# Performance work log

Hardware: AMD Instinct MI355X
Metric: run time of the kernel (lower is better)

## Reference

```python
import jax, jax.numpy as jnp
import numpy as np

TOP_K = 8
ROUTED_SCALING = 2.5


def setup_inputs() -> dict:
    key = jax.random.key(0)
    ks = jax.random.split(key, 8)
    B, S, H, E, I = 2, 1024, 2048, 32, 1024
    IS = 2 * I  # shared expert intermediate (n_shared_experts * moe_intermediate_size)
    w = lambda k, shape: jax.random.normal(k, shape, dtype=jnp.float32) * 0.02
    return {
        "hidden_states": jax.random.normal(ks[0], (B, S, H), dtype=jnp.float32),
        "gate_weight": w(ks[1], (E, H)),
        "w_gate": w(ks[2], (E, H, I)),
        "w_up": w(ks[3], (E, H, I)),
        "w_down": w(ks[4], (E, I, H)),
        "ws_gate": w(ks[5], (H, IS)),
        "ws_up": w(ks[6], (H, IS)),
        "ws_down": w(ks[7], (IS, H)),
    }


def reference(hidden_states, gate_weight, w_gate, w_up, w_down, ws_gate, ws_up, ws_down):
    B, S, H = hidden_states.shape
    x = hidden_states.reshape(-1, H)  # [T, H]
    T = x.shape[0]
    E = gate_weight.shape[0]

    # --- gate (DeepseekV3 top-k router: sigmoid scores, top-k, renormalize, scale) ---
    scores = jax.nn.sigmoid(x @ gate_weight.T)              # [T, E]
    topk_w, topk_i = jax.lax.top_k(scores, TOP_K)           # [T, K]
    topk_w = topk_w / (jnp.sum(topk_w, axis=-1, keepdims=True) + 1e-20)
    topk_w = topk_w * ROUTED_SCALING

    # dense [T, E] combine weights (scatter of top-k weights; zeros elsewhere)
    dense_w = jnp.zeros((T, E), dtype=topk_w.dtype).at[
        jnp.arange(T)[:, None], topk_i
    ].add(topk_w)

    # --- all experts on all tokens (calibrate_all_experts semantics; non-selected get weight 0) ---
    g = jnp.einsum('th,ehi->eti', x, w_gate)                # [E, T, I]
    u = jnp.einsum('th,ehi->eti', x, w_up)                  # [E, T, I]
    eo = jnp.einsum('eti,eih->eth', jax.nn.silu(g) * u, w_down)  # [E, T, H]
    routed = jnp.einsum('eth,te->th', eo, dense_w)          # weighted scatter-combine

    # --- shared expert (gated SiLU MLP on residual) ---
    shared = (jax.nn.silu(x @ ws_gate) * (x @ ws_up)) @ ws_down

    return (routed + shared).reshape(B, S, H)
```

## Files before the change

kernel.cpp:

```cpp
#include <hip/hip_runtime.h>

#define T_TOK 2048
#define H_DIM 2048
#define E_NUM 32
#define I_DIM 1024
#define IS_DIM 2048
#define K_TOT (E_NUM * I_DIM + IS_DIM)
#define SLOT_CAP 2048
#define NE_ALL 34
#define GU_TILES 192
#define DN_TILES 176
#define ACT_SLOTS 24576

typedef __bf16 bf16x8 __attribute__((ext_vector_type(8)));
typedef float  f32x4  __attribute__((ext_vector_type(4)));
static_assert(sizeof(bf16x8) == 16, "bf16x8 must be 16B");

#define OFF_CNT   ((size_t)0)
#define OFF_NTGU  ((size_t)192)
#define OFF_NTDN  ((size_t)196)
#define OFF_BASE  ((size_t)256)
#define OFF_TGU   ((size_t)512)
#define OFF_TDN   ((size_t)1280)
#define OFF_PAIRS ((size_t)2048)
#define OFF_XB    ((size_t)280576)
#define OFF_WGT   ((size_t)8669184)
#define OFF_WUT   ((size_t)142886912)
#define OFF_WSGT  ((size_t)277104640)
#define OFF_WSUT  ((size_t)285493248)
#define OFF_WDT   ((size_t)293881856)
#define OFF_ACT   ((size_t)436488192)

__device__ __forceinline__ unsigned short f2bf(float f) {
  unsigned int u = __float_as_uint(f);
  u += 0x7fffu + ((u >> 16) & 1u);
  return (unsigned short)(u >> 16);
}

__device__ __forceinline__ void gld16(const void* g, void* l) {
  __builtin_amdgcn_global_load_lds(
      (const __attribute__((address_space(1))) unsigned int*)g,
      (__attribute__((address_space(3))) unsigned int*)l, 16, 0, 0);
}

__global__ __launch_bounds__(256) void router_kernel(
    const float* __restrict__ x, const float* __restrict__ gw,
    int* __restrict__ cnt, unsigned int* __restrict__ pairs)
{
  const int t = blockIdx.x;
  __shared__ float xs[H_DIM];
  __shared__ float sc[E_NUM];
  const float4* xr = (const float4*)(x + (long)t * H_DIM);
  for (int i = threadIdx.x; i < H_DIM / 4; i += 256) ((float4*)xs)[i] = xr[i];
  __syncthreads();
  const int e = threadIdx.x >> 3, p = threadIdx.x & 7;
  const float4* ga = (const float4*)(gw + (long)e * H_DIM);
  const float4* xa = (const float4*)xs;
  float s = 0.f;
  #pragma unroll 4
  for (int i = p * 64; i < p * 64 + 64; ++i) {
    float4 a = ga[i], b = xa[i];
    s += a.x * b.x + a.y * b.y + a.z * b.z + a.w * b.w;
  }
  s += __shfl_down(s, 4, 8);
  s += __shfl_down(s, 2, 8);
  s += __shfl_down(s, 1, 8);
  if (p == 0) sc[e] = 1.f / (1.f + expf(-s));
  __syncthreads();
  if (threadIdx.x == 0) {
    float v[E_NUM];
    #pragma unroll
    for (int i = 0; i < E_NUM; ++i) v[i] = sc[i];
    unsigned mask = 0; float sum = 0.f;
    int sel[8]; float wv[8];
    for (int k = 0; k < 8; ++k) {
      float best = -1.f; int bi = 0;
      for (int i = 0; i < E_NUM; ++i)
        if (!((mask >> i) & 1u) && v[i] > best) { best = v[i]; bi = i; }
      mask |= 1u << bi; sel[k] = bi; wv[k] = best; sum += best;
    }
    const float scale = 2.5f / (sum + 1e-20f);
    for (int k = 0; k < 8; ++k) {
      const int slot = atomicAdd(&cnt[sel[k]], 1);
      if (slot < SLOT_CAP) {
        const unsigned int w16 = (unsigned int)f2bf(wv[k] * scale);
        pairs[sel[k] * SLOT_CAP + slot] = (w16 << 16) | (unsigned int)t;
      }
    }
  }
}

__global__ __launch_bounds__(256) void build_tiles_kernel(
    int* __restrict__ cnt, int* __restrict__ base,
    unsigned int* __restrict__ tgu, int* __restrict__ ntgu,
    unsigned int* __restrict__ tdn, int* __restrict__ ntdn,
    unsigned int* __restrict__ pairs)
{
  const int t = threadIdx.x;
  for (int s = t; s < T_TOK; s += 256) {
    const unsigned int pv = (0x3F80u << 16) | (unsigned int)s;
    pairs[32 * SLOT_CAP + s] = pv;
    pairs[33 * SLOT_CAP + s] = pv;
  }
  if (t == 0) {
    cnt[32] = T_TOK; cnt[33] = T_TOK;
    int b = 0, ngu = 0, ndn = 0;
    for (int e = 0; e < NE_ALL; ++e) {
      const int c = (e < 32) ? cnt[e] : T_TOK;
      base[e] = b;
      for (int m0 = 0; m0 < c; m0 += 128) {
        tgu[ngu++] = ((unsigned int)e << 16) | (unsigned int)m0;
        if (e < 33) tdn[ndn++] = ((unsigned int)e << 16) | (unsigned int)m0;
      }
      b += (c + 127) & ~127;
    }
    *ntgu = ngu; *ntdn = ndn;
  }
}

__global__ __launch_bounds__(256) void cvt_bf16_kernel(
    const float* __restrict__ in, unsigned short* __restrict__ out, int n4)
{
  int i = blockIdx.x * 256 + threadIdx.x;
  if (i >= n4) return;
  float4 v = ((const float4*)in)[i];
  ushort4 o;
  o.x = f2bf(v.x); o.y = f2bf(v.y); o.z = f2bf(v.z); o.w = f2bf(v.w);
  ((ushort4*)out)[i] = o;
}

struct TDescTable {
  const float* in[6];
  unsigned short* out[6];
  int C[6];
  int ldout[6];
  long in_bs[6];
  long out_bs[6];
  int nbx[6];
  int nbxy[6];
  int start[7];
};

__global__ __launch_bounds__(256) void transpose_fused(TDescTable td)
{
  const int bid = blockIdx.x;
  int i = 0;
  while (i < 5 && bid >= td.start[i + 1]) ++i;
  const int local = bid - td.start[i];
  const int bz = local / td.nbxy[i];
  const int rem = local % td.nbxy[i];
  const int by = rem / td.nbx[i];
  const int bx = rem % td.nbx[i];
  const float* in = td.in[i] + (long)bz * td.in_bs[i];
  unsigned short* out = td.out[i] + (long)bz * td.out_bs[i];
  const int C = td.C[i], ldout = td.ldout[i];

  __shared__ unsigned short tile[64][258];
  const int c0 = bx * 64;
  const int r0 = by * 256;
  const int t = threadIdx.x;
  const int rl0 = t >> 4;
  const int cl0 = (t & 15) * 4;
  #pragma unroll
  for (int p = 0; p < 16; ++p) {
    const int rl = p * 16 + rl0;
    float4 v = *(const float4*)(in + (long)(r0 + rl) * C + c0 + cl0);
    tile[cl0 + 0][rl] = f2bf(v.x);
    tile[cl0 + 1][rl] = f2bf(v.y);
    tile[cl0 + 2][rl] = f2bf(v.z);
    tile[cl0 + 3][rl] = f2bf(v.w);
  }
  __syncthreads();
  const int cw = t >> 5;
  const int rw = (t & 31) * 8;
  #pragma unroll
  for (int q = 0; q < 8; ++q) {
    const int cl = q * 8 + cw;
    const char* src = (const char*)&tile[cl][rw];
    uint4 o;
    o.x = *(const unsigned int*)(src + 0);
    o.y = *(const unsigned int*)(src + 4);
    o.z = *(const unsigned int*)(src + 8);
    o.w = *(const unsigned int*)(src + 12);
    *(uint4*)(out + (long)(c0 + cl) * ldout + r0 + rw) = o;
  }
}

__global__ __launch_bounds__(512, 4) void gate_up_moe_kernel(
    const unsigned short* __restrict__ xb,
    const unsigned short* __restrict__ bgT,
    const unsigned short* __restrict__ buT,
    const unsigned short* __restrict__ sgT,
    const unsigned short* __restrict__ suT,
    const int* __restrict__ cnt,
    const int* __restrict__ base,
    const unsigned int* __restrict__ pairs,
    const unsigned int* __restrict__ tiles,
    const int* __restrict__ ntp,
    unsigned short* __restrict__ act)
{
  const int ti = blockIdx.y;
  if (ti >= *ntp) return;
  const unsigned int tile = tiles[ti];
  const int e  = (int)(tile >> 16);
  const int m0 = (int)(tile & 0xFFFFu);
  const int cnte = cnt[e];
  const int be = base[e];
  const int n0 = blockIdx.x * 64;
  const long panel = (long)I_DIM * H_DIM;
  const unsigned short* Bg =
      ((e < 32) ? bgT + e * panel : sgT + (e - 32) * panel) + (long)n0 * H_DIM;
  const unsigned short* Bu =
      ((e < 32) ? buT + e * panel : suT + (e - 32) * panel) + (long)n0 * H_DIM;

  __shared__ unsigned short sA[2][128 * 64];
  __shared__ unsigned short sBg[2][64 * 64];
  __shared__ unsigned short sBu[2][64 * 64];

  const int tid = threadIdx.x;
  const int lane = tid & 63;
  const int wid = tid >> 6;
  const int wm = wid >> 1, wn = wid & 1;
  const int l15 = lane & 15;
  const int lk  = (lane >> 4) * 8;
  const int srow = tid >> 3;
  const int scol = (tid & 7) * 8;
  const int scolsw = (((tid & 7) ^ (srow & 7))) * 8;
  const int ksw = (l15 & 7) << 3;

  const unsigned short* asrc[2];
  #pragma unroll
  for (int r = 0; r < 2; ++r) {
    const int slot = m0 + r * 64 + srow;
    const unsigned int pr = (slot < cnte) ? pairs[e * SLOT_CAP + slot] : 0u;
    asrc[r] = xb + (long)(pr & 0xFFFFu) * H_DIM + scolsw;
  }

  const f32x4 fz = {0.f, 0.f, 0.f, 0.f};
  f32x4 accg[2][2], accu[2][2];
  #pragma unroll
  for (int i = 0; i < 2; ++i)
    #pragma unroll
    for (int j = 0; j < 2; ++j) { accg[i][j] = fz; accu[i][j] = fz; }

#define STAGE_GU(buf, k0) do {                                                 \
    gld16(asrc[0] + (k0), sA[buf] + srow * 64 + scol);                         \
    gld16(asrc[1] + (k0), sA[buf] + (64 + srow) * 64 + scol);                  \
    gld16(Bg + (long)srow * H_DIM + (k0) + scolsw,                             \
          sBg[buf] + srow * 64 + scol);                                        \
    gld16(Bu + (long)srow * H_DIM + (k0) + scolsw,                             \
          sBu[buf] + srow * 64 + scol);                                        \
  } while (0)

#define COMP_GU(buf) do {                                                      \
    _Pragma("unroll")                                                          \
    for (int kk = 0; kk < 2; ++kk) {                                           \
      const int ko = kk * 32 + lk;                                             \
      bf16x8 a[2], g[2], u[2];                                                 \
      _Pragma("unroll")                                                        \
      for (int mi = 0; mi < 2; ++mi)                                           \
        a[mi] = *(const bf16x8*)(sA[buf] + (wm * 32 + mi * 16 + l15) * 64 +    \
                                 (ko ^ ksw));                                  \
      _Pragma("unroll")                                                        \
      for (int ni = 0; ni < 2; ++ni) {                                         \
        g[ni] = *(const bf16x8*)(sBg[buf] + (wn * 32 + ni * 16 + l15) * 64 +   \
                                 (ko ^ ksw));                                  \
        u[ni] = *(const bf16x8*)(sBu[buf] + (wn * 32 + ni * 16 + l15) * 64 +   \
                                 (ko ^ ksw));                                  \
      }                                                                        \
      _Pragma("unroll")                                                        \
      for (int mi = 0; mi < 2; ++mi)                                           \
        _Pragma("unroll")                                                      \
        for (int ni = 0; ni < 2; ++ni) {                                       \
          accg[mi][ni] = __builtin_amdgcn_mfma_f32_16x16x32_bf16(              \
              a[mi], g[ni], accg[mi][ni], 0, 0, 0);                            \
          accu[mi][ni] = __builtin_amdgcn_mfma_f32_16x16x32_bf16(              \
              a[mi], u[ni], accu[mi][ni], 0, 0, 0);                            \
        }                                                                      \
    }                                                                          \
  } while (0)

  STAGE_GU(0, 0);
  __syncthreads();
  for (int t = 0; t < 32; t += 2) {
    if (t + 1 < 32) STAGE_GU(1, (t + 1) * 64);
    COMP_GU(0);
    __syncthreads();
    if (t + 2 < 32) STAGE_GU(0, (t + 2) * 64);
    COMP_GU(1);
    __syncthreads();
  }
#undef STAGE_GU
#undef COMP_GU

  const int colb = n0 + wn * 32;
  #pragma unroll
  for (int mi = 0; mi < 2; ++mi) {
    #pragma unroll
    for (int r = 0; r < 4; ++r) {
      const int slot = m0 + wm * 32 + mi * 16 + (lane >> 4) * 4 + r;
      if (slot < cnte) {
        const unsigned int pr = pairs[e * SLOT_CAP + slot];
        const float w = __uint_as_float(pr & 0xFFFF0000u);
        #pragma unroll
        for (int ni = 0; ni < 2; ++ni) {
          const float gv = accg[mi][ni][r];
          const float uv = accu[mi][ni][r];
          const float sv = (gv / (1.f + expf(-gv))) * uv * w;
          act[((long)(be + slot)) * I_DIM + colb + ni * 16 + l15] = f2bf(sv);
        }
      }
    }
  }
}

__global__ __launch_bounds__(512, 4) void down_moe_kernel(
    const unsigned short* __restrict__ act,
    const unsigned short* __restrict__ wdT,
    const int* __restrict__ cnt,
    const int* __restrict__ base,
    const unsigned int* __restrict__ pairs,
    const unsigned int* __restrict__ tiles,
    const int* __restrict__ ntp,
    float* __restrict__ out)
{
  const int ti = blockIdx.y;
  if (ti >= *ntp) return;
  const unsigned int tile = tiles[ti];
  const int e  = (int)(tile >> 16);
  const int m0 = (int)(tile & 0xFFFFu);
  const int cnte = cnt[e];
  const int n0 = blockIdx.x * 64;
  const unsigned short* A = act + ((long)base[e] + m0) * I_DIM;
  const unsigned short* B = wdT + (long)n0 * K_TOT + (long)e * I_DIM;
  const int nk = (e == 32) ? 32 : 16;

  __shared__ unsigned short sA[2][128 * 64];
  __shared__ unsigned short sB[2][64 * 64];

  const int tid = threadIdx.x;
  const int lane = tid & 63;
  const int wid = tid >> 6;
  const int wm = wid >> 1, wn = wid & 1;
  const int l15 = lane & 15;
  const int lk  = (lane >> 4) * 8;
  const int srow = tid >> 3;
  const int scol = (tid & 7) * 8;
  const int scolsw = (((tid & 7) ^ (srow & 7))) * 8;
  const int ksw = (l15 & 7) << 3;

  const f32x4 fz = {0.f, 0.f, 0.f, 0.f};
  f32x4 acc[2][2];
  #pragma unroll
  for (int i = 0; i < 2; ++i)
    #pragma unroll
    for (int j = 0; j < 2; ++j) acc[i][j] = fz;

#define STAGE_DN(buf, k0) do {                                                 \
    const long koff = (long)((k0) & 1023) +                                    \
                      (long)((k0) >> 10) * (2048L * 1024L);                    \
    gld16(A + (long)srow * I_DIM + koff + scolsw,                              \
          sA[buf] + srow * 64 + scol);                                         \
    gld16(A + (long)(64 + srow) * I_DIM + koff + scolsw,                       \
          sA[buf] + (64 + srow) * 64 + scol);                                  \
    gld16(B + (long)srow * K_TOT + (k0) + scolsw,                              \
          sB[buf] + srow * 64 + scol);                                         \
  } while (0)

#define COMP_DN(buf) do {                                                      \
    _Pragma("unroll")                                                          \
    for (int kk = 0; kk < 2; ++kk) {                                           \
      const int ko = kk * 32 + lk;                                             \
      bf16x8 a[2], b[2];                                                       \
      _Pragma("unroll")                                                        \
      for (int mi = 0; mi < 2; ++mi)                                           \
        a[mi] = *(const bf16x8*)(sA[buf] + (wm * 32 + mi * 16 + l15) * 64 +    \
                                 (ko ^ ksw));                                  \
      _Pragma("unroll")                                                        \
      for (int ni = 0; ni < 2; ++ni)                                           \
        b[ni] = *(const bf16x8*)(sB[buf] + (wn * 32 + ni * 16 + l15) * 64 +    \
                                 (ko ^ ksw));                                  \
      _Pragma("unroll")                                                        \
      for (int mi = 0; mi < 2; ++mi)                                           \
        _Pragma("unroll")                                                      \
        for (int ni = 0; ni < 2; ++ni)                                         \
          acc[mi][ni] = __builtin_amdgcn_mfma_f32_16x16x32_bf16(               \
              a[mi], b[ni], acc[mi][ni], 0, 0, 0);                             \
    }                                                                          \
  } while (0)

  STAGE_DN(0, 0);
  __syncthreads();
  for (int t = 0; t < nk; t += 2) {
    if (t + 1 < nk) STAGE_DN(1, (t + 1) * 64);
    COMP_DN(0);
    __syncthreads();
    if (t + 2 < nk) STAGE_DN(0, (t + 2) * 64);
    COMP_DN(1);
    __syncthreads();
  }
#undef STAGE_DN
#undef COMP_DN

  #pragma unroll
  for (int mi = 0; mi < 2; ++mi) {
    #pragma unroll
    for (int r = 0; r < 4; ++r) {
      const int slot = m0 + wm * 32 + mi * 16 + (lane >> 4) * 4 + r;
      if (slot < cnte) {
        const int tok = (int)(pairs[e * SLOT_CAP + slot] & 0xFFFFu);
        #pragma unroll
        for (int ni = 0; ni < 2; ++ni)
          atomicAdd(out + (long)tok * H_DIM + n0 + wn * 32 + ni * 16 + l15,
                    acc[mi][ni][r]);
      }
    }
  }
}

extern "C" void kernel_launch(void* const* d_in, const int* in_sizes, int n_in,
                              void* d_out, int out_size, void* d_ws, size_t ws_size,
                              hipStream_t stream) {
  (void)in_sizes; (void)n_in; (void)ws_size;
  const float* x   = (const float*)d_in[0];
  const float* gw  = (const float*)d_in[1];
  const float* wg  = (const float*)d_in[2];
  const float* wu  = (const float*)d_in[3];
  const float* wd  = (const float*)d_in[4];
  const float* wsg = (const float*)d_in[5];
  const float* wsu = (const float*)d_in[6];
  const float* wsd = (const float*)d_in[7];
  float* out = (float*)d_out;
  char* ws = (char*)d_ws;

  int*            cnt   = (int*)(ws + OFF_CNT);
  int*            ntgu  = (int*)(ws + OFF_NTGU);
  int*            ntdn  = (int*)(ws + OFF_NTDN);
  int*            basep = (int*)(ws + OFF_BASE);
  unsigned int*   tgu   = (unsigned int*)(ws + OFF_TGU);
  unsigned int*   tdn   = (unsigned int*)(ws + OFF_TDN);
  unsigned int*   pairs = (unsigned int*)(ws + OFF_PAIRS);
  unsigned short* xb    = (unsigned short*)(ws + OFF_XB);
  unsigned short* wgT   = (unsigned short*)(ws + OFF_WGT);
  unsigned short* wuT   = (unsigned short*)(ws + OFF_WUT);
  unsigned short* wsgT  = (unsigned short*)(ws + OFF_WSGT);
  unsigned short* wsuT  = (unsigned short*)(ws + OFF_WSUT);
  unsigned short* wdT   = (unsigned short*)(ws + OFF_WDT);
  unsigned short* actb  = (unsigned short*)(ws + OFF_ACT);

  hipMemsetAsync(ws + OFF_CNT, 0, 256, stream);
  hipMemsetAsync(out, 0, (size_t)out_size * sizeof(float), stream);

  router_kernel<<<T_TOK, 256, 0, stream>>>(x, gw, cnt, pairs);
  build_tiles_kernel<<<1, 256, 0, stream>>>(cnt, basep, tgu, ntgu, tdn, ntdn,
                                            pairs);
  cvt_bf16_kernel<<<(T_TOK * H_DIM / 4 + 255) / 256, 256, 0, stream>>>(
      x, xb, T_TOK * H_DIM / 4);

  TDescTable td;
  td.in[0] = wg;  td.out[0] = wgT;  td.C[0] = I_DIM;  td.ldout[0] = H_DIM;
  td.in_bs[0] = (long)H_DIM * I_DIM; td.out_bs[0] = (long)I_DIM * H_DIM;
  td.nbx[0] = I_DIM / 64; td.nbxy[0] = (I_DIM / 64) * (H_DIM / 256);
  td.in[1] = wu;  td.out[1] = wuT;  td.C[1] = I_DIM;  td.ldout[1] = H_DIM;
  td.in_bs[1] = (long)H_DIM * I_DIM; td.out_bs[1] = (long)I_DIM * H_DIM;
  td.nbx[1] = I_DIM / 64; td.nbxy[1] = (I_DIM / 64) * (H_DIM / 256);
  td.in[2] = wd;  td.out[2] = wdT;  td.C[2] = H_DIM;  td.ldout[2] = K_TOT;
  td.in_bs[2] = (long)I_DIM * H_DIM; td.out_bs[2] = (long)I_DIM;
  td.nbx[2] = H_DIM / 64; td.nbxy[2] = (H_DIM / 64) * (I_DIM / 256);
  td.in[3] = wsg; td.out[3] = wsgT; td.C[3] = IS_DIM; td.ldout[3] = H_DIM;
  td.in_bs[3] = 0; td.out_bs[3] = 0;
  td.nbx[3] = IS_DIM / 64; td.nbxy[3] = (IS_DIM / 64) * (H_DIM / 256);
  td.in[4] = wsu; td.out[4] = wsuT; td.C[4] = IS_DIM; td.ldout[4] = H_DIM;
  td.in_bs[4] = 0; td.out_bs[4] = 0;
  td.nbx[4] = IS_DIM / 64; td.nbxy[4] = (IS_DIM / 64) * (H_DIM / 256);
  td.in[5] = wsd; td.out[5] = wdT + E_NUM * I_DIM; td.C[5] = H_DIM;
  td.ldout[5] = K_TOT; td.in_bs[5] = 0; td.out_bs[5] = 0;
  td.nbx[5] = H_DIM / 64; td.nbxy[5] = (H_DIM / 64) * (IS_DIM / 256);
  td.start[0] = 0;
  for (int i = 0; i < 5; ++i) {
    int nz = (i <= 2) ? E_NUM : 1;
    td.start[i + 1] = td.start[i] + td.nbxy[i] * nz;
  }
  td.start[6] = td.start[5] + td.nbxy[5];
  transpose_fused<<<td.start[6], 256, 0, stream>>>(td);

  gate_up_moe_kernel<<<dim3(16, GU_TILES), 512, 0, stream>>>(
      xb, wgT, wuT, wsgT, wsuT, cnt, basep, pairs, tgu, ntgu, actb);

  down_moe_kernel<<<dim3(32, DN_TILES), 512, 0, stream>>>(
      actb, wdT, cnt, basep, pairs, tdn, ntdn, out);
}
```

Measured before the change: 860.9 us.

## Fuse fp32-to-bf16 weight transpose into MoE GEMM loaders

```diff
diff --git a/kernel.cpp b/kernel.cpp
--- a/kernel.cpp
+++ b/kernel.cpp
@@ -5,7 +5,6 @@
 #define E_NUM 32
 #define I_DIM 1024
 #define IS_DIM 2048
-#define K_TOT (E_NUM * I_DIM + IS_DIM)
 #define SLOT_CAP 2048
 #define NE_ALL 34
 #define GU_TILES 192
@@ -24,17 +23,18 @@
 #define OFF_TDN   ((size_t)1280)
 #define OFF_PAIRS ((size_t)2048)
 #define OFF_XB    ((size_t)280576)
-#define OFF_WGT   ((size_t)8669184)
-#define OFF_WUT   ((size_t)142886912)
-#define OFF_WSGT  ((size_t)277104640)
-#define OFF_WSUT  ((size_t)285493248)
-#define OFF_WDT   ((size_t)293881856)
-#define OFF_ACT   ((size_t)436488192)
+#define OFF_ACT   ((size_t)8669184)
 
 __device__ __forceinline__ unsigned short f2bf(float f) {
   unsigned int u = __float_as_uint(f);
   u += 0x7fffu + ((u >> 16) & 1u);
   return (unsigned short)(u >> 16);
+}
+
+__device__ __forceinline__ unsigned int cvtpk(float lo, float hi) {
+  unsigned int r;
+  asm volatile("v_cvt_pk_bf16_f32 %0, %1, %2" : "=v"(r) : "v"(lo), "v"(hi));
+  return r;
 }
 
 __device__ __forceinline__ void gld16(const void* g, void* l) {
@@ -129,69 +129,12 @@
   ((ushort4*)out)[i] = o;
 }
 
-struct TDescTable {
-  const float* in[6];
-  unsigned short* out[6];
-  int C[6];
-  int ldout[6];
-  long in_bs[6];
-  long out_bs[6];
-  int nbx[6];
-  int nbxy[6];
-  int start[7];
-};
-
-__global__ __launch_bounds__(256) void transpose_fused(TDescTable td)
-{
-  const int bid = blockIdx.x;
-  int i = 0;
-  while (i < 5 && bid >= td.start[i + 1]) ++i;
-  const int local = bid - td.start[i];
-  const int bz = local / td.nbxy[i];
-  const int rem = local % td.nbxy[i];
-  const int by = rem / td.nbx[i];
-  const int bx = rem % td.nbx[i];
-  const float* in = td.in[i] + (long)bz * td.in_bs[i];
-  unsigned short* out = td.out[i] + (long)bz * td.out_bs[i];
-  const int C = td.C[i], ldout = td.ldout[i];
-
-  __shared__ unsigned short tile[64][258];
-  const int c0 = bx * 64;
-  const int r0 = by * 256;
-  const int t = threadIdx.x;
-  const int rl0 = t >> 4;
-  const int cl0 = (t & 15) * 4;
-  #pragma unroll
-  for (int p = 0; p < 16; ++p) {
-    const int rl = p * 16 + rl0;
-    float4 v = *(const float4*)(in + (long)(r0 + rl) * C + c0 + cl0);
-    tile[cl0 + 0][rl] = f2bf(v.x);
-    tile[cl0 + 1][rl] = f2bf(v.y);
-    tile[cl0 + 2][rl] = f2bf(v.z);
-    tile[cl0 + 3][rl] = f2bf(v.w);
-  }
-  __syncthreads();
-  const int cw = t >> 5;
-  const int rw = (t & 31) * 8;
-  #pragma unroll
-  for (int q = 0; q < 8; ++q) {
-    const int cl = q * 8 + cw;
-    const char* src = (const char*)&tile[cl][rw];
-    uint4 o;
-    o.x = *(const unsigned int*)(src + 0);
-    o.y = *(const unsigned int*)(src + 4);
-    o.z = *(const unsigned int*)(src + 8);
-    o.w = *(const unsigned int*)(src + 12);
-    *(uint4*)(out + (long)(c0 + cl) * ldout + r0 + rw) = o;
-  }
-}
-
-__global__ __launch_bounds__(512, 4) void gate_up_moe_kernel(
+__global__ __launch_bounds__(512, 3) void gate_up_moe_kernel(
     const unsigned short* __restrict__ xb,
-    const unsigned short* __restrict__ bgT,
-    const unsigned short* __restrict__ buT,
-    const unsigned short* __restrict__ sgT,
-    const unsigned short* __restrict__ suT,
+    const float* __restrict__ wg,
+    const float* __restrict__ wu,
+    const float* __restrict__ wsg,
+    const float* __restrict__ wsu,
     const int* __restrict__ cnt,
     const int* __restrict__ base,
     const unsigned int* __restrict__ pairs,
@@ -207,11 +150,16 @@
   const int cnte = cnt[e];
   const int be = base[e];
   const int n0 = blockIdx.x * 64;
-  const long panel = (long)I_DIM * H_DIM;
-  const unsigned short* Bg =
-      ((e < 32) ? bgT + e * panel : sgT + (e - 32) * panel) + (long)n0 * H_DIM;
-  const unsigned short* Bu =
-      ((e < 32) ? buT + e * panel : suT + (e - 32) * panel) + (long)n0 * H_DIM;
+  const float* Bg; const float* Bu; long ldB;
+  if (e < 32) {
+    Bg = wg + (long)e * H_DIM * I_DIM + n0;
+    Bu = wu + (long)e * H_DIM * I_DIM + n0;
+    ldB = I_DIM;
+  } else {
+    Bg = wsg + (e - 32) * I_DIM + n0;
+    Bu = wsu + (e - 32) * I_DIM + n0;
+    ldB = IS_DIM;
+  }
 
   __shared__ unsigned short sA[2][128 * 64];
   __shared__ unsigned short sBg[2][64 * 64];
@@ -225,8 +173,11 @@
   const int lk  = (lane >> 4) * 8;
   const int srow = tid >> 3;
   const int scol = (tid & 7) * 8;
-  const int scolsw = (((tid & 7) ^ (srow & 7))) * 8;
+  const int scolsw = ((tid & 7) ^ (srow & 7)) * 8;
   const int ksw = (l15 & 7) << 3;
+
+  const int kA = ((tid & 15) | ((tid >> 8) << 4)) * 2;
+  const int cA = ((tid >> 4) & 15) * 4;
 
   const unsigned short* asrc[2];
   #pragma unroll
@@ -243,13 +194,30 @@
     #pragma unroll
     for (int j = 0; j < 2; ++j) { accg[i][j] = fz; accu[i][j] = fz; }
 
-#define STAGE_GU(buf, k0) do {                                                 \
+  float4 vg0, vg1, vu0, vu1;
+
+#define LOADB_GU(k0) do {                                                      \
+    const float* bg = Bg + (long)((k0) + kA) * ldB + cA;                       \
+    const float* bu = Bu + (long)((k0) + kA) * ldB + cA;                       \
+    vg0 = *(const float4*)bg; vg1 = *(const float4*)(bg + ldB);                \
+    vu0 = *(const float4*)bu; vu1 = *(const float4*)(bu + ldB);                \
+  } while (0)
+
+#define WRITEB_GU(buf) do {                                                    \
+    _Pragma("unroll")                                                          \
+    for (int j = 0; j < 4; ++j) {                                              \
+      const int n = cA + j;                                                    \
+      const int li = n * 64 + (((kA >> 3) ^ (n & 7)) << 3) + (kA & 7);         \
+      *(unsigned int*)&sBg[buf][li] =                                          \
+          cvtpk(((const float*)&vg0)[j], ((const float*)&vg1)[j]);             \
+      *(unsigned int*)&sBu[buf][li] =                                          \
+          cvtpk(((const float*)&vu0)[j], ((const float*)&vu1)[j]);             \
+    }                                                                          \
+  } while (0)
+
+#define STAGEA_GU(buf, k0) do {                                                \
     gld16(asrc[0] + (k0), sA[buf] + srow * 64 + scol);                         \
     gld16(asrc[1] + (k0), sA[buf] + (64 + srow) * 64 + scol);                  \
-    gld16(Bg + (long)srow * H_DIM + (k0) + scolsw,                             \
-          sBg[buf] + srow * 64 + scol);                                        \
-    gld16(Bu + (long)srow * H_DIM + (k0) + scolsw,                             \
-          sBu[buf] + srow * 64 + scol);                                        \
   } while (0)
 
 #define COMP_GU(buf) do {                                                      \
@@ -280,17 +248,20 @@
     }                                                                          \
   } while (0)
 
-  STAGE_GU(0, 0);
+  LOADB_GU(0);
+  STAGEA_GU(0, 0);
+  WRITEB_GU(0);
   __syncthreads();
-  for (int t = 0; t < 32; t += 2) {
-    if (t + 1 < 32) STAGE_GU(1, (t + 1) * 64);
-    COMP_GU(0);
+  for (int t = 0; t < 32; ++t) {
+    const int cur = t & 1, nxt = cur ^ 1;
+    if (t < 31) { LOADB_GU((t + 1) * 64); STAGEA_GU(nxt, (t + 1) * 64); }
+    COMP_GU(cur);
+    if (t < 31) WRITEB_GU(nxt);
     __syncthreads();
-    if (t + 2 < 32) STAGE_GU(0, (t + 2) * 64);
-    COMP_GU(1);
-    __syncthreads();
-  }
-#undef STAGE_GU
+  }
+#undef LOADB_GU
+#undef WRITEB_GU
+#undef STAGEA_GU
 #undef COMP_GU
 
   const int colb = n0 + wn * 32;
@@ -314,9 +285,10 @@
   }
 }
 
-__global__ __launch_bounds__(512, 4) void down_moe_kernel(
+__global__ __launch_bounds__(512, 3) void down_moe_kernel(
     const unsigned short* __restrict__ act,
-    const unsigned short* __restrict__ wdT,
+    const float* __restrict__ wd,
+    const float* __restrict__ wsd,
     const int* __restrict__ cnt,
     const int* __restrict__ base,
     const unsigned int* __restrict__ pairs,
@@ -332,7 +304,7 @@
   const int cnte = cnt[e];
   const int n0 = blockIdx.x * 64;
   const unsigned short* A = act + ((long)base[e] + m0) * I_DIM;
-  const unsigned short* B = wdT + (long)n0 * K_TOT + (long)e * I_DIM;
+  const float* B = (e < 32) ? wd + (long)e * I_DIM * H_DIM + n0 : wsd + n0;
   const int nk = (e == 32) ? 32 : 16;
 
   __shared__ unsigned short sA[2][128 * 64];
@@ -346,8 +318,11 @@
   const int lk  = (lane >> 4) * 8;
   const int srow = tid >> 3;
   const int scol = (tid & 7) * 8;
-  const int scolsw = (((tid & 7) ^ (srow & 7))) * 8;
+  const int scolsw = ((tid & 7) ^ (srow & 7)) * 8;
   const int ksw = (l15 & 7) << 3;
+
+  const int kA = ((tid & 15) | ((tid >> 8) << 4)) * 2;
+  const int cA = ((tid >> 4) & 15) * 4;
 
   const f32x4 fz = {0.f, 0.f, 0.f, 0.f};
   f32x4 acc[2][2];
@@ -356,15 +331,30 @@
     #pragma unroll
     for (int j = 0; j < 2; ++j) acc[i][j] = fz;
 
-#define STAGE_DN(buf, k0) do {                                                 \
+  float4 vb0, vb1;
+
+#define LOADB_DN(k0) do {                                                      \
+    const float* bp = B + (long)((k0) + kA) * H_DIM + cA;                      \
+    vb0 = *(const float4*)bp; vb1 = *(const float4*)(bp + H_DIM);              \
+  } while (0)
+
+#define WRITEB_DN(buf) do {                                                    \
+    _Pragma("unroll")                                                          \
+    for (int j = 0; j < 4; ++j) {                                              \
+      const int n = cA + j;                                                    \
+      const int li = n * 64 + (((kA >> 3) ^ (n & 7)) << 3) + (kA & 7);         \
+      *(unsigned int*)&sB[buf][li] =                                           \
+          cvtpk(((const float*)&vb0)[j], ((const float*)&vb1)[j]);             \
+    }                                                                          \
+  } while (0)
+
+#define STAGEA_DN(buf, k0) do {                                                \
     const long koff = (long)((k0) & 1023) +                                    \
                       (long)((k0) >> 10) * (2048L * 1024L);                    \
     gld16(A + (long)srow * I_DIM + koff + scolsw,                              \
           sA[buf] + srow * 64 + scol);                                         \
     gld16(A + (long)(64 + srow) * I_DIM + koff + scolsw,                       \
           sA[buf] + (64 + srow) * 64 + scol);                                  \
-    gld16(B + (long)srow * K_TOT + (k0) + scolsw,                              \
-          sB[buf] + srow * 64 + scol);                                         \
   } while (0)
 
 #define COMP_DN(buf) do {                                                      \
@@ -389,17 +379,20 @@
     }                                                                          \
   } while (0)
 
-  STAGE_DN(0, 0);
+  LOADB_DN(0);
+  STAGEA_DN(0, 0);
+  WRITEB_DN(0);
   __syncthreads();
-  for (int t = 0; t < nk; t += 2) {
-    if (t + 1 < nk) STAGE_DN(1, (t + 1) * 64);
-    COMP_DN(0);
+  for (int t = 0; t < nk; ++t) {
+    const int cur = t & 1, nxt = cur ^ 1;
+    if (t < nk - 1) { LOADB_DN((t + 1) * 64); STAGEA_DN(nxt, (t + 1) * 64); }
+    COMP_DN(cur);
+    if (t < nk - 1) WRITEB_DN(nxt);
     __syncthreads();
-    if (t + 2 < nk) STAGE_DN(0, (t + 2) * 64);
-    COMP_DN(1);
-    __syncthreads();
-  }
-#undef STAGE_DN
+  }
+#undef LOADB_DN
+#undef WRITEB_DN
+#undef STAGEA_DN
 #undef COMP_DN
 
   #pragma unroll
@@ -441,11 +434,6 @@
   unsigned int*   tdn   = (unsigned int*)(ws + OFF_TDN);
   unsigned int*   pairs = (unsigned int*)(ws + OFF_PAIRS);
   unsigned short* xb    = (unsigned short*)(ws + OFF_XB);
-  unsigned short* wgT   = (unsigned short*)(ws + OFF_WGT);
-  unsigned short* wuT   = (unsigned short*)(ws + OFF_WUT);
-  unsigned short* wsgT  = (unsigned short*)(ws + OFF_WSGT);
-  unsigned short* wsuT  = (unsigned short*)(ws + OFF_WSUT);
-  unsigned short* wdT   = (unsigned short*)(ws + OFF_WDT);
   unsigned short* actb  = (unsigned short*)(ws + OFF_ACT);
 
   hipMemsetAsync(ws + OFF_CNT, 0, 256, stream);
@@ -457,36 +445,9 @@
   cvt_bf16_kernel<<<(T_TOK * H_DIM / 4 + 255) / 256, 256, 0, stream>>>(
       x, xb, T_TOK * H_DIM / 4);
 
-  TDescTable td;
-  td.in[0] = wg;  td.out[0] = wgT;  td.C[0] = I_DIM;  td.ldout[0] = H_DIM;
-  td.in_bs[0] = (long)H_DIM * I_DIM; td.out_bs[0] = (long)I_DIM * H_DIM;
-  td.nbx[0] = I_DIM / 64; td.nbxy[0] = (I_DIM / 64) * (H_DIM / 256);
-  td.in[1] = wu;  td.out[1] = wuT;  td.C[1] = I_DIM;  td.ldout[1] = H_DIM;
-  td.in_bs[1] = (long)H_DIM * I_DIM; td.out_bs[1] = (long)I_DIM * H_DIM;
-  td.nbx[1] = I_DIM / 64; td.nbxy[1] = (I_DIM / 64) * (H_DIM / 256);
-  td.in[2] = wd;  td.out[2] = wdT;  td.C[2] = H_DIM;  td.ldout[2] = K_TOT;
-  td.in_bs[2] = (long)I_DIM * H_DIM; td.out_bs[2] = (long)I_DIM;
-  td.nbx[2] = H_DIM / 64; td.nbxy[2] = (H_DIM / 64) * (I_DIM / 256);
-  td.in[3] = wsg; td.out[3] = wsgT; td.C[3] = IS_DIM; td.ldout[3] = H_DIM;
-  td.in_bs[3] = 0; td.out_bs[3] = 0;
-  td.nbx[3] = IS_DIM / 64; td.nbxy[3] = (IS_DIM / 64) * (H_DIM / 256);
-  td.in[4] = wsu; td.out[4] = wsuT; td.C[4] = IS_DIM; td.ldout[4] = H_DIM;
-  td.in_bs[4] = 0; td.out_bs[4] = 0;
-  td.nbx[4] = IS_DIM / 64; td.nbxy[4] = (IS_DIM / 64) * (H_DIM / 256);
-  td.in[5] = wsd; td.out[5] = wdT + E_NUM * I_DIM; td.C[5] = H_DIM;
-  td.ldout[5] = K_TOT; td.in_bs[5] = 0; td.out_bs[5] = 0;
-  td.nbx[5] = H_DIM / 64; td.nbxy[5] = (H_DIM / 64) * (IS_DIM / 256);
-  td.start[0] = 0;
-  for (int i = 0; i < 5; ++i) {
-    int nz = (i <= 2) ? E_NUM : 1;
-    td.start[i + 1] = td.start[i] + td.nbxy[i] * nz;
-  }
-  td.start[6] = td.start[5] + td.nbxy[5];
-  transpose_fused<<<td.start[6], 256, 0, stream>>>(td);
-
   gate_up_moe_kernel<<<dim3(16, GU_TILES), 512, 0, stream>>>(
-      xb, wgT, wuT, wsgT, wsuT, cnt, basep, pairs, tgu, ntgu, actb);
+      xb, wg, wu, wsg, wsu, cnt, basep, pairs, tgu, ntgu, actb);
 
   down_moe_kernel<<<dim3(32, DN_TILES), 512, 0, stream>>>(
-      actb, wdT, cnt, basep, pairs, tdn, ntdn, out);
-}
+      actb, wd, wsd, cnt, basep, pairs, tdn, ntdn, out);
+}
```

Result: slower. 936.9 us (+8.8%).
